# Performance work log

Measured on AMD Instinct MI355X. Metric: run time of the kernel, lower is better.

Reference implementation:

```python
import jax, jax.numpy as jnp
import numpy as np
from jax import lax

DN = ('NCHW', 'OIHW', 'NCHW')

def _conv(x, w, b, stride, pad):
    y = lax.conv_general_dilated(x, w, (stride, stride), [(pad, pad), (pad, pad)], dimension_numbers=DN)
    return y + b[None, :, None, None]

def _resblock(x, w1, b1, w2, b2, wd, bd, stride):
    # standard pre-activation-free ResNet block: conv3x3(stride)-ReLU-conv3x3 + 1x1(stride) skip, final ReLU
    identity = _conv(x, wd, bd, stride, 0)
    h = jax.nn.relu(_conv(x, w1, b1, stride, 1))
    h = _conv(h, w2, b2, 1, 1)
    return jax.nn.relu(h + identity)

def _deconv(x, w, b, stride, out_pad):
    # PyTorch ConvTranspose2d(k=3, padding=1, output_padding=out_pad) as dilated conv
    # w has PyTorch layout (in_ch, out_ch, kH, kW) -> flip spatially, swap to OIHW
    wt = jnp.flip(w, (2, 3)).transpose(1, 0, 2, 3)
    y = lax.conv_general_dilated(x, wt, (1, 1), [(1, 1 + out_pad), (1, 1 + out_pad)], lhs_dilation=(stride, stride), dimension_numbers=DN)
    return y + b[None, :, None, None]

def _quantize(enc, codebook):
    # enc: (B, C, H, W); codebook: (N, C). Squared-Euclidean distances, argmin, lookup.
    e = enc.transpose(0, 2, 3, 1)  # (B, H, W, C)
    d = (jnp.sum(e * e, axis=-1, keepdims=True)
         - 2.0 * jnp.einsum('bhwc,nc->bhwn', e, codebook)
         + jnp.sum(codebook * codebook, axis=-1))  # (B, H, W, N)
    idx = jnp.argmin(d, axis=-1)
    q = codebook[idx]  # (B, H, W, C)
    return q.transpose(0, 3, 1, 2)

def setup_inputs() -> dict:
    key = jax.random.key(0)
    ks = jax.random.split(key, 28)
    def W(k, shape):
        return jax.random.normal(k, shape, jnp.float32) * 0.05
    inp = {"x": jax.random.normal(ks[0], (32, 3, 256, 256), jnp.float32)}
    enc_chans = [(3, 64), (64, 128), (128, 64)]
    i = 1
    for l, (cin, cout) in enumerate(enc_chans):
        inp[f"enc{l}_w1"] = W(ks[i], (cout, cin, 3, 3))
        inp[f"enc{l}_b1"] = W(ks[i + 1], (cout,))
        inp[f"enc{l}_w2"] = W(ks[i + 2], (cout, cout, 3, 3))
        inp[f"enc{l}_b2"] = W(ks[i + 3], (cout,))
        inp[f"enc{l}_wd"] = W(ks[i + 4], (cout, cin, 1, 1))
        inp[f"enc{l}_bd"] = W(ks[i + 5], (cout,))
        i += 6
    # decoder ConvTranspose2d weights in PyTorch layout (in_ch, out_ch, 3, 3)
    dec_chans = [(64, 128), (128, 64), (64, 3)]
    for l, (cin, cout) in enumerate(dec_chans):
        inp[f"dec{l}_w"] = W(ks[i], (cin, cout, 3, 3))
        inp[f"dec{l}_b"] = W(ks[i + 1], (cout,))
        i += 2
    inp["codebook"] = W(ks[i], (512, 64))
    return inp

def reference(x, enc0_w1, enc0_b1, enc0_w2, enc0_b2, enc0_wd, enc0_bd,
              enc1_w1, enc1_b1, enc1_w2, enc1_b2, enc1_wd, enc1_bd,
              enc2_w1, enc2_b1, enc2_w2, enc2_b2, enc2_wd, enc2_bd,
              dec0_w, dec0_b, dec1_w, dec1_b, dec2_w, dec2_b, codebook):
    # encode: 256 -> 128 -> 64 -> 64 spatially
    h = _resblock(x, enc0_w1, enc0_b1, enc0_w2, enc0_b2, enc0_wd, enc0_bd, 2)
    h = _resblock(h, enc1_w1, enc1_b1, enc1_w2, enc1_b2, enc1_wd, enc1_bd, 2)
    h = _resblock(h, enc2_w1, enc2_b1, enc2_w2, enc2_b2, enc2_wd, enc2_bd, 1)
    q = _quantize(h, codebook)
    # decode with output_size matching encoder input shapes (output_padding: 0, 1, 1)
    h = jax.nn.relu(_deconv(q, dec0_w, dec0_b, 1, 0))   # 64 -> 64
    h = jax.nn.relu(_deconv(h, dec1_w, dec1_b, 2, 1))   # 64 -> 128
    return _deconv(h, dec2_w, dec2_b, 2, 1)             # 128 -> 256
```

## Files before the change

### kernel.cpp

```cpp
#include <hip/hip_runtime.h>
#include <cstddef>


typedef float v4f __attribute__((ext_vector_type(4)));
typedef _Float16 f16x8 __attribute__((ext_vector_type(8)));
typedef _Float16 f16x4 __attribute__((ext_vector_type(4)));

__device__ __forceinline__ void fma4(v4f& a, float p, const v4f& w) {
    a.x = fmaf(p, w.x, a.x); a.y = fmaf(p, w.y, a.y);
    a.z = fmaf(p, w.z, a.z); a.w = fmaf(p, w.w, a.w);
}

__global__ void repack_k(const float* __restrict__ src, float* __restrict__ dst,
                         int cout, int coutR, int cin, int flip, int deconv)
{
    int t = blockIdx.x * 256 + threadIdx.x;
    int tot = cin * 9 * cout;
    if (t >= tot) return;
    int co = t % cout; int k = (t / cout) % 9; int ci = t / (9 * cout);
    float v = 0.f;
    if (co < coutR) {
        int ks = flip ? 8 - k : k;
        v = deconv ? src[((size_t)ci * coutR + co) * 9 + ks]
                   : src[((size_t)co * cin + ci) * 9 + ks];
    }
    dst[t] = v;
}

__global__ void repackB16_k(const float* __restrict__ src, _Float16* __restrict__ bh,
                            _Float16* __restrict__ bl, int COUT, int CIN, int deconv)
{
    int t = blockIdx.x * 256 + threadIdx.x;
    int tot = 9 * CIN * COUT;
    if (t >= tot) return;
    int NGtot = COUT >> 4, C32 = CIN >> 5;
    int j = t & 7;
    int lane = (t >> 3) & 63;
    int blk = t >> 9;
    int ng = blk % NGtot; blk /= NGtot;
    int c32 = blk % C32;
    int tap = blk / C32;
    int co = ng * 16 + (lane & 15);
    int ci = c32 * 32 + ((lane >> 4) & 3) * 8 + j;
    float v = deconv ? src[((size_t)ci * COUT + co) * 9 + (8 - tap)]
                     : src[((size_t)co * CIN + ci) * 9 + tap];
    _Float16 h = (_Float16)v;
    _Float16 l = (_Float16)(v - (float)h);
    bh[t] = h; bl[t] = l;
}

__global__ void repackQ_k(const float* __restrict__ cb, _Float16* __restrict__ qb)
{
    int t = blockIdx.x * 256 + threadIdx.x;
    if (t >= 65536) return;
    int j = t & 7;
    int lane = (t >> 3) & 63;
    int hl = (t >> 9) & 1;
    int s = (t >> 10) & 1;
    int nt = t >> 11;
    int code = nt * 16 + (lane & 15);
    int ci = s * 32 + ((lane >> 4) & 3) * 8 + j;
    float v = cb[(size_t)code * 64 + ci];
    _Float16 h = (_Float16)v;
    qb[t] = hl ? (_Float16)(v - (float)h) : h;
}

__global__ void cbnorm_k(const float* __restrict__ cb, float* __restrict__ cn)
{
    int i = blockIdx.x * 256 + threadIdx.x;
    if (i >= 512) return;
    float s = 0.f;
#pragma unroll
    for (int j = 0; j < 64; ++j) { float v = cb[i * 64 + j]; s = fmaf(v, v, s); }
    cn[i] = s;
}

template<int CIN, bool RELU, int ADDMODE, bool CLIN, bool CLOUT>
__launch_bounds__(256, 2)
__global__ void mconv3s1_k(const float* __restrict__ in,
                           const _Float16* __restrict__ Bh, const _Float16* __restrict__ Bl,
                           const float* __restrict__ bias, float* __restrict__ out,
                           const float* __restrict__ addend,
                           int COUT, int H, int W)
{
    constexpr int C32 = CIN / 32;
    __shared__ __align__(16) unsigned char smBuf[76416];
    _Float16* AH = (_Float16*)smBuf;
    _Float16* AL = AH + 12960;
    _Float16* BW = AL + 12960;
    float* smO = (float*)smBuf;

    const int tid = threadIdx.x;
    const int lane = tid & 63, yb = tid >> 6;
    const int n16 = lane & 15, q = lane >> 4;

    int b = blockIdx.x;
    const int chunks = COUT >> 6;
    const int coch = b % chunks; b /= chunks;
    const int tX = W >> 4; const int tx = b % tX; b /= tX;
    const int tY = H >> 4; const int ty = b % tY; const int n = b / tY;
    const int x0 = tx * 16, y0 = ty * 16;
    const int NGtot = COUT >> 4;
    const int ngbase = coch * 4, cobase = coch * 64;

    v4f acc[4][4];
#pragma unroll
    for (int ng = 0; ng < 4; ++ng) {
        float bb = bias[cobase + ng * 16 + n16];
        v4f bv = {bb, bb, bb, bb};
#pragma unroll
        for (int mg = 0; mg < 4; ++mg) acc[mg][ng] = bv;
    }

    for (int c32 = 0; c32 < C32; ++c32) {
        __syncthreads();
        if (CLIN) {
            for (int u = tid; u < 2592; u += 256) {
                int cell = u >> 3, f4 = u & 7;
                int yy = cell / 18, xx = cell - yy * 18;
                int gy = y0 - 1 + yy, gx = x0 - 1 + xx;
                float4 v = make_float4(0.f, 0.f, 0.f, 0.f);
                if (gy >= 0 && gy < H && gx >= 0 && gx < W)
                    v = *(const float4*)&in[(((size_t)n * H + gy) * W + gx) * CIN + c32 * 32 + f4 * 4];
                f16x4 h4, l4;
                h4[0] = (_Float16)v.x; l4[0] = (_Float16)(v.x - (float)h4[0]);
                h4[1] = (_Float16)v.y; l4[1] = (_Float16)(v.y - (float)h4[1]);
                h4[2] = (_Float16)v.z; l4[2] = (_Float16)(v.z - (float)h4[2]);
                h4[3] = (_Float16)v.w; l4[3] = (_Float16)(v.w - (float)h4[3]);
                int a = (yy * 18 + xx) * 40 + f4 * 4;
                *(f16x4*)&AH[a] = h4; *(f16x4*)&AL[a] = l4;
            }
        } else {
            for (int u = tid; u < 10368; u += 256) {
                int ci = u / 324, rem = u - ci * 324;
                int yy = rem / 18, xx = rem - yy * 18;
                int gy = y0 - 1 + yy, gx = x0 - 1 + xx;
                float v = 0.f;
                if (gy >= 0 && gy < H && gx >= 0 && gx < W)
                    v = in[(((size_t)n * CIN + c32 * 32 + ci) * H + gy) * W + gx];
                _Float16 h = (_Float16)v;
                _Float16 l = (_Float16)(v - (float)h);
                int a = (yy * 18 + xx) * 40 + ci;
                AH[a] = h; AL[a] = l;
            }
        }
        for (int ky = 0; ky < 3; ++ky) {
            __syncthreads();
            for (int u = tid; u < 1536; u += 256) {
                int lu = u & 63;
                int rest = u >> 6;
                int hl = rest & 1; rest >>= 1;
                int ng = rest & 3;
                int tapL = rest >> 2;
                const uint4* srcp = (const uint4*)(hl ? Bl : Bh);
                size_t sidx = (((size_t)(ky * 3 + tapL) * C32 + c32) * NGtot + ngbase + ng) * 64 + lu;
                ((uint4*)BW)[u] = srcp[sidx];
            }
            __syncthreads();
#pragma unroll
            for (int kx = 0; kx < 3; ++kx) {
                f16x8 aH[4], aL[4];
#pragma unroll
                for (int mg = 0; mg < 4; ++mg) {
                    int aoff = ((4 * yb + mg + ky) * 18 + n16 + kx) * 40 + q * 8;
                    aH[mg] = *(const f16x8*)&AH[aoff];
                    aL[mg] = *(const f16x8*)&AL[aoff];
                }
                __builtin_amdgcn_s_setprio(1);
#pragma unroll
                for (int ng = 0; ng < 4; ++ng) {
                    int boff = ((kx * 4 + ng) * 2) * 512 + lane * 8;
                    f16x8 bH = *(const f16x8*)&BW[boff];
                    f16x8 bL = *(const f16x8*)&BW[boff + 512];
#pragma unroll
                    for (int mg = 0; mg < 4; ++mg) {
                        acc[mg][ng] = __builtin_amdgcn_mfma_f32_16x16x32_f16(aH[mg], bH, acc[mg][ng], 0, 0, 0);
                        acc[mg][ng] = __builtin_amdgcn_mfma_f32_16x16x32_f16(aL[mg], bH, acc[mg][ng], 0, 0, 0);
                        acc[mg][ng] = __builtin_amdgcn_mfma_f32_16x16x32_f16(aH[mg], bL, acc[mg][ng], 0, 0, 0);
                    }
                }
                __builtin_amdgcn_s_setprio(0);
            }
        }
    }

    __syncthreads();
#pragma unroll
    for (int mg = 0; mg < 4; ++mg)
#pragma unroll
        for (int ng = 0; ng < 4; ++ng) {
            int p = (4 * yb + mg) * 16 + q * 4;
            int co = ng * 16 + n16;
#pragma unroll
            for (int r = 0; r < 4; ++r)
                smO[co * 257 + p + r] = acc[mg][ng][r];
        }
    __syncthreads();
    if (CLOUT) {
        const int p = tid;
        const int py = p >> 4, px = p & 15;
        size_t cellBase = (((size_t)n * H + (y0 + py)) * W + (x0 + px)) * COUT + cobase;
        float* cellp = out + cellBase;
        const float* acell = (ADDMODE == 2) ? addend + cellBase : nullptr;
#pragma unroll
        for (int g = 0; g < 16; ++g) {
            float4 v;
            v.x = smO[(4 * g + 0) * 257 + p];
            v.y = smO[(4 * g + 1) * 257 + p];
            v.z = smO[(4 * g + 2) * 257 + p];
            v.w = smO[(4 * g + 3) * 257 + p];
            if (ADDMODE == 2) {
                float4 a4 = *(const float4*)&acell[4 * g];
                v.x += a4.x; v.y += a4.y; v.z += a4.z; v.w += a4.w;
            }
            if (RELU) {
                v.x = fmaxf(v.x, 0.f); v.y = fmaxf(v.y, 0.f);
                v.z = fmaxf(v.z, 0.f); v.w = fmaxf(v.w, 0.f);
            }
            *(float4*)&cellp[4 * g] = v;
        }
    } else {
        const size_t plane = (size_t)H * W;
        float* ob = out + ((size_t)n * COUT + cobase) * plane;
        const float* ab = (ADDMODE == 1) ? addend + ((size_t)n * COUT + cobase) * plane : nullptr;
#pragma unroll
        for (int k = 0; k < 64; ++k) {
            int e = tid + 256 * k;
            int co = e >> 8, p = e & 255;
            int py = p >> 4, px = p & 15;
            size_t g = (size_t)co * plane + (size_t)(y0 + py) * W + x0 + px;
            float v = smO[co * 257 + p];
            if (ADDMODE == 1) v += ab[g];
            if (RELU) v = fmaxf(v, 0.f);
            ob[g] = v;
        }
    }
}

template<int CIN, int NG, bool RELU>
__launch_bounds__(256, 3)
__global__ void mconv3s2_k(const float* __restrict__ in,
                           const _Float16* __restrict__ Bh, const _Float16* __restrict__ Bl,
                           const float* __restrict__ bias, float* __restrict__ out,
                           int COUT, int Hin, int Win)
{
    constexpr int C32 = CIN / 32;
    constexpr int ASZ = 9 * 2 * 17 * 40;
    __shared__ __align__(16) unsigned char smBuf[2 * ASZ * 2];
    _Float16* AH = (_Float16*)smBuf;
    _Float16* AL = AH + ASZ;
    float* smO = (float*)smBuf;

    const int tid = threadIdx.x;
    const int lane = tid & 63, yb = tid >> 6;
    const int n16 = lane & 15, q = lane >> 4;

    const int Hout = Hin >> 1, Wout = Win >> 1;
    int b = blockIdx.x;
    const int chunks = COUT / (NG * 16);
    const int coch = b % chunks; b /= chunks;
    const int tX = Wout >> 4; const int tx = b % tX; b /= tX;
    const int tY = Hout >> 2; const int ty = b % tY; const int n = b / tY;
    const int x0 = tx * 16, y0 = ty * 4;
    const int gx0 = 2 * x0 - 1, gy0 = 2 * y0 - 1;
    const int NGtot = COUT >> 4;
    const int ngbase = coch * NG, cobase = coch * NG * 16;

    v4f acc[NG];
#pragma unroll
    for (int ng = 0; ng < NG; ++ng) {
        float bb = bias[cobase + ng * 16 + n16];
        v4f bv = {bb, bb, bb, bb};
        acc[ng] = bv;
    }

    const uint4* bhp = (const uint4*)Bh;
    const uint4* blp = (const uint4*)Bl;

    for (int c32 = 0; c32 < C32; ++c32) {
        __syncthreads();
        for (int u = tid; u < 2376; u += 256) {
            int cell = u >> 3, f4 = u & 7;
            int yy = cell / 33, xx = cell - yy * 33;
            int gy = gy0 + yy, gx = gx0 + xx;
            float4 v = make_float4(0.f, 0.f, 0.f, 0.f);
            if (gy >= 0 && gy < Hin && gx >= 0 && gx < Win)
                v = *(const float4*)&in[(((size_t)n * Hin + gy) * Win + gx) * CIN + c32 * 32 + f4 * 4];
            f16x4 h4, l4;
            h4[0] = (_Float16)v.x; l4[0] = (_Float16)(v.x - (float)h4[0]);
            h4[1] = (_Float16)v.y; l4[1] = (_Float16)(v.y - (float)h4[1]);
            h4[2] = (_Float16)v.z; l4[2] = (_Float16)(v.z - (float)h4[2]);
            h4[3] = (_Float16)v.w; l4[3] = (_Float16)(v.w - (float)h4[3]);
            int a = ((yy * 2 + (xx & 1)) * 17 + (xx >> 1)) * 40 + f4 * 4;
            *(f16x4*)&AH[a] = h4; *(f16x4*)&AL[a] = l4;
        }
        __syncthreads();
#pragma unroll
        for (int ky = 0; ky < 3; ++ky) {
#pragma unroll
            for (int kx = 0; kx < 3; ++kx) {
                const int par = kx & 1, xs = kx >> 1;
                int aoff = (((2 * yb + ky) * 2 + par) * 17 + n16 + xs) * 40 + q * 8;
                f16x8 aH = *(const f16x8*)&AH[aoff];
                f16x8 aL = *(const f16x8*)&AL[aoff];
                size_t sb0 = (((size_t)(ky * 3 + kx) * C32 + c32) * NGtot + ngbase) * 64 + lane;
                __builtin_amdgcn_s_setprio(1);
#pragma unroll
                for (int ng = 0; ng < NG; ++ng) {
                    uint4 rH = bhp[sb0 + (size_t)ng * 64];
                    uint4 rL = blp[sb0 + (size_t)ng * 64];
                    f16x8 bH = *(const f16x8*)&rH;
                    f16x8 bL = *(const f16x8*)&rL;
                    acc[ng] = __builtin_amdgcn_mfma_f32_16x16x32_f16(aH, bH, acc[ng], 0, 0, 0);
                    acc[ng] = __builtin_amdgcn_mfma_f32_16x16x32_f16(aL, bH, acc[ng], 0, 0, 0);
                    acc[ng] = __builtin_amdgcn_mfma_f32_16x16x32_f16(aH, bL, acc[ng], 0, 0, 0);
                }
                __builtin_amdgcn_s_setprio(0);
            }
        }
    }

    __syncthreads();
#pragma unroll
    for (int ng = 0; ng < NG; ++ng) {
        int co = ng * 16 + n16;
        int p = yb * 16 + q * 4;
#pragma unroll
        for (int r = 0; r < 4; ++r)
            smO[co * 65 + p + r] = acc[ng][r];
    }
    __syncthreads();
    const int p2 = tid >> 2, s2 = tid & 3;
    const int py = p2 >> 4, px = p2 & 15;
    float* cellp = out + ((((size_t)n * Hout + (y0 + py)) * Wout + (x0 + px)) * COUT + s2 * 32);
#pragma unroll
    for (int k = 0; k < 8; ++k) {
        float4 v;
        v.x = smO[(s2 * 32 + 4 * k + 0) * 65 + p2];
        v.y = smO[(s2 * 32 + 4 * k + 1) * 65 + p2];
        v.z = smO[(s2 * 32 + 4 * k + 2) * 65 + p2];
        v.w = smO[(s2 * 32 + 4 * k + 3) * 65 + p2];
        if (RELU) {
            v.x = fmaxf(v.x, 0.f); v.y = fmaxf(v.y, 0.f);
            v.z = fmaxf(v.z, 0.f); v.w = fmaxf(v.w, 0.f);
        }
        *(float4*)&cellp[4 * k] = v;
    }
}

template<int CIN, bool RELU>
__launch_bounds__(256, 3)
__global__ void mdeconv2_k(const float* __restrict__ in,
                           const _Float16* __restrict__ Bh, const _Float16* __restrict__ Bl,
                           const float* __restrict__ bias, float* __restrict__ out,
                           int COUT, int Hin, int Win)
{
    constexpr int C32 = CIN / 32;
    __shared__ __align__(16) unsigned char smBuf[38976];
    _Float16* AH = (_Float16*)smBuf;
    _Float16* AL = AH + 3600;
    _Float16* BW = AL + 3600;
    float* smO = (float*)smBuf;

    const int tid = threadIdx.x;
    const int lane = tid & 63, yb = tid >> 6;
    const int n16 = lane & 15, q = lane >> 4;

    int b = blockIdx.x;
    const int chunks = COUT >> 6;
    const int coch = b % chunks; b /= chunks;
    const int tX = Win >> 4; const int tx = b % tX; b /= tX;
    const int tY = Hin >> 2; const int ty = b % tY; const int n = b / tY;
    const int x0 = tx * 16, y0 = ty * 4;
    const int NGtot = COUT >> 4;
    const int ngbase = coch * 4, cobase = coch * 64;

    v4f acc[4][4];
#pragma unroll
    for (int ng = 0; ng < 4; ++ng) {
        float bb = bias[cobase + ng * 16 + n16];
        v4f bv = {bb, bb, bb, bb};
#pragma unroll
        for (int ph = 0; ph < 4; ++ph) acc[ph][ng] = bv;
    }

    for (int c32 = 0; c32 < C32; ++c32) {
        __syncthreads();
        for (int u = tid; u < 680; u += 256) {
            int cell = u >> 3, f4 = u & 7;
            int yy = cell / 17, xx = cell - yy * 17;
            int gy = y0 + yy, gx = x0 + xx;
            float4 v = make_float4(0.f, 0.f, 0.f, 0.f);
            if (gy < Hin && gx < Win)
                v = *(const float4*)&in[(((size_t)n * Hin + gy) * Win + gx) * CIN + c32 * 32 + f4 * 4];
            f16x4 h4, l4;
            h4[0] = (_Float16)v.x; l4[0] = (_Float16)(v.x - (float)h4[0]);
            h4[1] = (_Float16)v.y; l4[1] = (_Float16)(v.y - (float)h4[1]);
            h4[2] = (_Float16)v.z; l4[2] = (_Float16)(v.z - (float)h4[2]);
            h4[3] = (_Float16)v.w; l4[3] = (_Float16)(v.w - (float)h4[3]);
            int a = (yy * 18 + xx) * 40 + f4 * 4;
            *(f16x4*)&AH[a] = h4; *(f16x4*)&AL[a] = l4;
        }
        for (int ky = 0; ky < 3; ++ky) {
            __syncthreads();
            for (int u = tid; u < 1536; u += 256) {
                int lu = u & 63;
                int rest = u >> 6;
                int hl = rest & 1; rest >>= 1;
                int ng = rest & 3;
                int tapL = rest >> 2;
                const uint4* srcp = (const uint4*)(hl ? Bl : Bh);
                size_t sidx = (((size_t)(ky * 3 + tapL) * C32 + c32) * NGtot + ngbase + ng) * 64 + lu;
                ((uint4*)BW)[u] = srcp[sidx];
            }
            __syncthreads();
            const int iy = (ky == 2) ? 1 : 0;
            const int phy = (ky == 1) ? 0 : 2;
#pragma unroll
            for (int kx = 0; kx < 3; ++kx) {
                const int ix = (kx == 2) ? 1 : 0;
                const int ph = phy + ((kx == 1) ? 0 : 1);
                int aoff = ((yb + iy) * 18 + n16 + ix) * 40 + q * 8;
                f16x8 aH = *(const f16x8*)&AH[aoff];
                f16x8 aL = *(const f16x8*)&AL[aoff];
                __builtin_amdgcn_s_setprio(1);
#pragma unroll
                for (int ng = 0; ng < 4; ++ng) {
                    int boff = ((kx * 4 + ng) * 2) * 512 + lane * 8;
                    f16x8 bH = *(const f16x8*)&BW[boff];
                    f16x8 bL = *(const f16x8*)&BW[boff + 512];
                    acc[ph][ng] = __builtin_amdgcn_mfma_f32_16x16x32_f16(aH, bH, acc[ph][ng], 0, 0, 0);
                    acc[ph][ng] = __builtin_amdgcn_mfma_f32_16x16x32_f16(aL, bH, acc[ph][ng], 0, 0, 0);
                    acc[ph][ng] = __builtin_amdgcn_mfma_f32_16x16x32_f16(aH, bL, acc[ph][ng], 0, 0, 0);
                }
                __builtin_amdgcn_s_setprio(0);
            }
        }
    }

    const int Wout = Win * 2;
    const size_t plane = (size_t)(Hin * 2) * (size_t)Wout;
    float* ob = out + ((size_t)n * COUT + cobase) * plane;
    const int oy0 = 2 * y0, ox0 = 2 * x0;
#pragma unroll
    for (int half = 0; half < 2; ++half) {
        __syncthreads();
#pragma unroll
        for (int ph = 0; ph < 4; ++ph) {
            const int dy = ph >> 1, dx = ph & 1;
#pragma unroll
            for (int g = 0; g < 2; ++g) {
                int ng = half * 2 + g;
#pragma unroll
                for (int r = 0; r < 4; ++r)
                    smO[(g * 16 + n16) * 257 + (2 * yb + dy) * 32 + 2 * (q * 4 + r) + dx] = acc[ph][ng][r];
            }
        }
        __syncthreads();
#pragma unroll
        for (int k = 0; k < 32; ++k) {
            int pos = tid;
            int oyl = pos >> 5, oxl = pos & 31;
            float v = smO[k * 257 + pos];
            if (RELU) v = fmaxf(v, 0.f);
            ob[(size_t)(half * 32 + k) * plane + (size_t)(oy0 + oyl) * Wout + ox0 + oxl] = v;
        }
    }
}

template<int CIN, int CB, bool RELU>
__launch_bounds__(256, 4)
__global__ void conv3s2_k(const float* __restrict__ in, const float* __restrict__ wp,
                          const float* __restrict__ bias, float* __restrict__ out,
                          int COUT, int Hin, int Win)
{
    constexpr int COC = 32;
    __shared__ float smIn[CB * 2178];
    __shared__ float smW[CB * 9 * COC];
    const int Hout = Hin >> 1, Wout = Win >> 1;
    const int tid = threadIdx.x;
    int b = blockIdx.x;
    const int chunks = COUT / COC;
    const int tX = Wout / 32, tY = Hout / 16;
    const int ch = b % chunks; b /= chunks;
    const int tx = b % tX; b /= tX;
    const int ty = b % tY; const int n = b / tY;
    const int cobase = ch * COC;
    const int r = tid >> 4, c = tid & 15;
    const int gy0 = ty * 32 - 1, gx0 = tx * 64 - 1;

    v4f acc[16];
#pragma unroll
    for (int g = 0; g < 8; ++g) {
        v4f bv = *(const v4f*)&bias[cobase + 4 * g];
        acc[g] = bv; acc[8 + g] = bv;
    }

    const size_t plane = (size_t)Hin * Win;
    const float* ip0 = in + (size_t)n * CIN * plane;
    const float* wp0 = wp + cobase;

    for (int ci0 = 0; ci0 < CIN; ci0 += CB) {
        __syncthreads();
        for (int idx = tid; idx < CB * 2178; idx += 256) {
            int ci = idx / 2178, rem = idx - ci * 2178;
            int rr = rem / 66, cc = rem - rr * 66;
            int gy = gy0 + rr, gx = gx0 + cc;
            float v = 0.f;
            if (gy >= 0 && gy < Hin && gx >= 0 && gx < Win)
                v = ip0[(size_t)(ci0 + ci) * plane + (size_t)gy * Win + gx];
            smIn[idx] = v;
        }
        for (int idx = tid; idx < CB * 9 * COC; idx += 256) {
            int q2 = idx >> 5, co = idx & 31;
            smW[idx] = wp0[((size_t)ci0 * 9 + q2) * COUT + co];
        }
        __syncthreads();

#pragma unroll 1
        for (int ci = 0; ci < CB; ++ci) {
            float p[15];
            const float* sp = &smIn[ci * 2178 + 2 * r * 66 + 4 * c];
#pragma unroll
            for (int i = 0; i < 3; ++i)
#pragma unroll
                for (int j = 0; j < 5; ++j)
                    p[i * 5 + j] = sp[i * 66 + j];
            const float* wrow = &smW[ci * 288];
#pragma unroll
            for (int k = 0; k < 9; ++k) {
                const int ky = k / 3, kx = k % 3;
#pragma unroll
                for (int g = 0; g < 8; ++g) {
                    v4f wv = *(const v4f*)&wrow[k * 32 + 4 * g];
                    fma4(acc[g],     p[ky * 5 + kx],     wv);
                    fma4(acc[8 + g], p[ky * 5 + kx + 2], wv);
                }
            }
        }
    }

    const int oy = ty * 16 + r, ox = tx * 32 + 2 * c;
    size_t cellBase = (((size_t)n * Hout + oy) * Wout + ox) * COUT + cobase;
#pragma unroll
    for (int g = 0; g < 8; ++g) {
        v4f v0 = acc[g], v1 = acc[8 + g];
        if (RELU) {
#pragma unroll
            for (int e = 0; e < 4; ++e) { v0[e] = fmaxf(v0[e], 0.f); v1[e] = fmaxf(v1[e], 0.f); }
        }
        *(v4f*)&out[cellBase + 4 * g] = v0;
        *(v4f*)&out[cellBase + COUT + 4 * g] = v1;
    }
}

template<int CIN, int CB, int COC, bool RELU>
__launch_bounds__(256, 3)
__global__ void deconv2_k(const float* __restrict__ in, const float* __restrict__ wp,
                          const float* __restrict__ bias, float* __restrict__ out,
                          int COUTR, int COUTP, int Hin, int Win)
{
    constexpr int RW = 33, RH = 17;
    __shared__ float smIn[CB * RH * RW];
    __shared__ float smW[CB * 9 * COC];
    const int Wout = Win * 2;
    const int tid = threadIdx.x;
    int b = blockIdx.x;
    const int chunks = COUTP / COC;
    const int qTX = Win / 32, qTY = Hin / 16;
    const int ch = b % chunks; b /= chunks;
    const int qtx = b % qTX; b /= qTX;
    const int qty = b % qTY; const int n = b / qTY;
    const int cobase = ch * COC;
    const int tqy = tid >> 4, tqx = tid & 15;
    const int qby = qty * 16, qbx = qtx * 32;

    v4f acc[8 * COC / 4];
#pragma unroll
    for (int g = 0; g < COC / 4; ++g) {
        v4f bv;
#pragma unroll
        for (int e = 0; e < 4; ++e)
            bv[e] = (cobase + 4 * g + e < COUTR) ? bias[cobase + 4 * g + e] : 0.f;
#pragma unroll
        for (int pt = 0; pt < 8; ++pt) acc[pt * (COC / 4) + g] = bv;
    }

    const size_t plane = (size_t)Hin * Win;
    const float* ip0 = in + (size_t)n * CIN * plane;
    const float* wp0 = wp + cobase;

    for (int ci0 = 0; ci0 < CIN; ci0 += CB) {
        __syncthreads();
        for (int idx = tid; idx < CB * RH * RW; idx += 256) {
            int ci = idx / (RH * RW), rem = idx - ci * (RH * RW);
            int rr = rem / RW, cc = rem - rr * RW;
            int gy = qby + rr, gx = qbx + cc;
            float v = 0.f;
            if (gy < Hin && gx < Win)
                v = ip0[(size_t)(ci0 + ci) * plane + (size_t)gy * Win + gx];
            smIn[idx] = v;
        }
        for (int idx = tid; idx < CB * 9 * COC; idx += 256) {
            int q2 = idx / COC, co = idx % COC;
            smW[idx] = wp0[((size_t)ci0 * 9 + q2) * COUTP + co];
        }
        __syncthreads();

#pragma unroll 1
        for (int ci = 0; ci < CB; ++ci) {
            float p[6];
            const float* sp = &smIn[ci * RH * RW + tqy * RW + 2 * tqx];
#pragma unroll
            for (int i = 0; i < 2; ++i)
#pragma unroll
                for (int j = 0; j < 3; ++j)
                    p[i * 3 + j] = sp[i * RW + j];
            const float* wrow = &smW[ci * 9 * COC];
#pragma unroll
            for (int k = 0; k < 9; ++k) {
                const int ky = k / 3, kx = k % 3;
                const int dy = (ky == 1) ? 0 : 1, iy = (ky == 0) ? 1 : 0;
                const int dx = (kx == 1) ? 0 : 1, ix = (kx == 0) ? 1 : 0;
#pragma unroll
                for (int g = 0; g < COC / 4; ++g) {
                    v4f wv = *(const v4f*)&wrow[k * COC + 4 * g];
                    fma4(acc[(0 + dy * 2 + dx) * (COC / 4) + g], p[iy * 3 + ix],     wv);
                    fma4(acc[(4 + dy * 2 + dx) * (COC / 4) + g], p[iy * 3 + ix + 1], wv);
                }
            }
        }
    }

    const size_t oPlane = (size_t)(Hin * 2) * Wout;
    const int oy = 2 * (qby + tqy), ox = 2 * (qbx + 2 * tqx);
#pragma unroll
    for (int g = 0; g < COC / 4; ++g)
#pragma unroll
        for (int e = 0; e < 4; ++e) {
            int cch = cobase + 4 * g + e;
            if (cch >= COUTR) break;
            float* op = out + ((size_t)n * COUTR + cch) * oPlane + (size_t)oy * Wout + ox;
#pragma unroll
            for (int a2 = 0; a2 < 2; ++a2) {
                float u0 = acc[(0 + a2 * 2 + 0) * (COC / 4) + g][e];
                float u1 = acc[(0 + a2 * 2 + 1) * (COC / 4) + g][e];
                float u2 = acc[(4 + a2 * 2 + 0) * (COC / 4) + g][e];
                float u3 = acc[(4 + a2 * 2 + 1) * (COC / 4) + g][e];
                if (RELU) { u0 = fmaxf(u0, 0.f); u1 = fmaxf(u1, 0.f);
                            u2 = fmaxf(u2, 0.f); u3 = fmaxf(u3, 0.f); }
                *(float4*)&op[(size_t)a2 * Wout] = make_float4(u0, u1, u2, u3);
            }
        }
}

template<int CIN, int S, bool RELU, bool CLIN, bool CLOUT>
__launch_bounds__(256, 4)
__global__ void conv1x1_k(const float* __restrict__ in, const float* __restrict__ w,
                          const float* __restrict__ bias, float* __restrict__ out,
                          int COUT, int Hin, int Win, int Hout, int Wout)
{
    constexpr int COC = 32;
    __shared__ float smW[CIN * COC];
    const int tid = threadIdx.x;
    int b = blockIdx.x;
    const int chunks = COUT / COC;
    const int spB = (Hout * Wout) / 256;
    const int ch = b % chunks; b /= chunks;
    const int sb = b % spB; const int n = b / spB;
    const int cobase = ch * COC;

    for (int idx = tid; idx < CIN * COC; idx += 256) {
        int ci = idx / COC, co = idx - ci * COC;
        smW[idx] = w[(size_t)(cobase + co) * CIN + ci];
    }
    __syncthreads();

    const int pos = sb * 256 + tid;
    const int oy = pos / Wout, ox = pos - oy * Wout;

    v4f acc[8];
#pragma unroll
    for (int g = 0; g < 8; ++g) acc[g] = *(const v4f*)&bias[cobase + 4 * g];

    if (CLIN) {
        const float* ip = in + (((size_t)n * Hin + oy * S) * Win + ox * S) * CIN;
#pragma unroll 1
        for (int c4 = 0; c4 < CIN / 4; ++c4) {
            v4f v = *(const v4f*)&ip[c4 * 4];
#pragma unroll
            for (int e = 0; e < 4; ++e)
#pragma unroll
                for (int g = 0; g < 8; ++g)
                    fma4(acc[g], v[e], *(const v4f*)&smW[(c4 * 4 + e) * COC + 4 * g]);
        }
    } else {
        const size_t inPlane = (size_t)Hin * Win;
        const float* ip = in + (size_t)n * CIN * inPlane + (size_t)(oy * S) * Win + (size_t)(ox * S);
#pragma unroll 1
        for (int ci = 0; ci < CIN; ++ci) {
            float v = ip[(size_t)ci * inPlane];
#pragma unroll
            for (int g = 0; g < 8; ++g)
                fma4(acc[g], v, *(const v4f*)&smW[ci * COC + 4 * g]);
        }
    }
    const size_t outPlane = (size_t)Hout * Wout;
    if (CLOUT) {
        size_t cb2 = ((size_t)n * outPlane + pos) * COUT + cobase;
#pragma unroll
        for (int g = 0; g < 8; ++g) {
            v4f v = acc[g];
            if (RELU) {
#pragma unroll
                for (int e = 0; e < 4; ++e) v[e] = fmaxf(v[e], 0.f);
            }
            *(v4f*)&out[cb2 + 4 * g] = v;
        }
    } else {
        float* op = out + ((size_t)n * COUT + cobase) * outPlane + pos;
#pragma unroll
        for (int g = 0; g < 8; ++g)
#pragma unroll
            for (int e = 0; e < 4; ++e) {
                float v = acc[g][e];
                if (RELU) v = fmaxf(v, 0.f);
                op[(size_t)(4 * g + e) * outPlane] = v;
            }
    }
}

__launch_bounds__(256, 4)
__global__ void mquant_k(const float* __restrict__ h, const _Float16* __restrict__ QB,
                         const float* __restrict__ cn, const float* __restrict__ cb,
                         float* __restrict__ q)
{
    __shared__ __align__(16) _Float16 AF[2][8192];
    __shared__ float cns[512];
    __shared__ int bidxs[128];

    const int tid = threadIdx.x;
    const int lane = tid & 63;
    const int wv = tid >> 6;
    const int n16 = lane & 15, qq = lane >> 4;

    const int n = blockIdx.x >> 5;
    const int rem0 = (blockIdx.x & 31) << 7;

    for (int u = tid; u < 1024; u += 256) {
        int posL = u >> 3, grp = u & 7;
        const float* gp = h + ((size_t)n * 4096 + rem0 + posL) * 64 + grp * 8;
        float4 v0 = *(const float4*)gp;
        float4 v1 = *(const float4*)(gp + 4);
        f16x8 hh, ll;
        hh[0] = (_Float16)v0.x; ll[0] = (_Float16)(v0.x - (float)hh[0]);
        hh[1] = (_Float16)v0.y; ll[1] = (_Float16)(v0.y - (float)hh[1]);
        hh[2] = (_Float16)v0.z; ll[2] = (_Float16)(v0.z - (float)hh[2]);
        hh[3] = (_Float16)v0.w; ll[3] = (_Float16)(v0.w - (float)hh[3]);
        hh[4] = (_Float16)v1.x; ll[4] = (_Float16)(v1.x - (float)hh[4]);
        hh[5] = (_Float16)v1.y; ll[5] = (_Float16)(v1.y - (float)hh[5]);
        hh[6] = (_Float16)v1.z; ll[6] = (_Float16)(v1.z - (float)hh[6]);
        hh[7] = (_Float16)v1.w; ll[7] = (_Float16)(v1.w - (float)hh[7]);
        int mt = posL >> 4, s = grp >> 2, qv = grp & 3;
        int a = ((mt * 2 + s) * 64 + (posL & 15) + qv * 16) * 8;
        *(f16x8*)&AF[0][a] = hh;
        *(f16x8*)&AF[1][a] = ll;
    }
    for (int u = tid; u < 512; u += 256) cns[u] = cn[u];
    __syncthreads();

    f16x8 aH[2][2], aL[2][2];
#pragma unroll
    for (int m = 0; m < 2; ++m)
#pragma unroll
        for (int s = 0; s < 2; ++s) {
            int a = (((wv * 2 + m) * 2 + s) * 64 + lane) * 8;
            aH[m][s] = *(const f16x8*)&AF[0][a];
            aL[m][s] = *(const f16x8*)&AF[1][a];
        }

    float best[2][4]; int bi[2][4];
#pragma unroll
    for (int m = 0; m < 2; ++m)
#pragma unroll
        for (int r = 0; r < 4; ++r) { best[m][r] = 3.4e38f; bi[m][r] = 0; }

    const uint4* qbp = (const uint4*)QB;
#pragma unroll 1
    for (int nt = 0; nt < 32; ++nt) {
        uint4 rH0 = qbp[((nt * 2 + 0) * 2 + 0) * 64 + lane];
        uint4 rL0 = qbp[((nt * 2 + 0) * 2 + 1) * 64 + lane];
        uint4 rH1 = qbp[((nt * 2 + 1) * 2 + 0) * 64 + lane];
        uint4 rL1 = qbp[((nt * 2 + 1) * 2 + 1) * 64 + lane];
        f16x8 bH0 = *(const f16x8*)&rH0;
        f16x8 bL0 = *(const f16x8*)&rL0;
        f16x8 bH1 = *(const f16x8*)&rH1;
        f16x8 bL1 = *(const f16x8*)&rL1;
        float cnv = cns[nt * 16 + n16];
        const int code = nt * 16 + n16;
        __builtin_amdgcn_s_setprio(1);
#pragma unroll
        for (int m = 0; m < 2; ++m) {
            v4f acc = {0.f, 0.f, 0.f, 0.f};
            acc = __builtin_amdgcn_mfma_f32_16x16x32_f16(aH[m][0], bH0, acc, 0, 0, 0);
            acc = __builtin_amdgcn_mfma_f32_16x16x32_f16(aL[m][0], bH0, acc, 0, 0, 0);
            acc = __builtin_amdgcn_mfma_f32_16x16x32_f16(aH[m][0], bL0, acc, 0, 0, 0);
            acc = __builtin_amdgcn_mfma_f32_16x16x32_f16(aH[m][1], bH1, acc, 0, 0, 0);
            acc = __builtin_amdgcn_mfma_f32_16x16x32_f16(aL[m][1], bH1, acc, 0, 0, 0);
            acc = __builtin_amdgcn_mfma_f32_16x16x32_f16(aH[m][1], bL1, acc, 0, 0, 0);
#pragma unroll
            for (int r = 0; r < 4; ++r) {
                float d = fmaf(-2.f, acc[r], cnv);
                if (d < best[m][r]) { best[m][r] = d; bi[m][r] = code; }
            }
        }
        __builtin_amdgcn_s_setprio(0);
    }

#pragma unroll
    for (int m = 0; m < 2; ++m)
#pragma unroll
        for (int r = 0; r < 4; ++r) {
#pragma unroll
            for (int msk = 1; msk < 16; msk <<= 1) {
                float ob = __shfl_xor(best[m][r], msk);
                int oi = __shfl_xor(bi[m][r], msk);
                if (ob < best[m][r] || (ob == best[m][r] && oi < bi[m][r])) {
                    best[m][r] = ob; bi[m][r] = oi;
                }
            }
            if (n16 == 0) bidxs[wv * 32 + m * 16 + qq * 4 + r] = bi[m][r];
        }
    __syncthreads();

    const int p = tid & 127, jh = tid >> 7;
    const int code = bidxs[p];
    const float4* crow4 = (const float4*)(cb + (size_t)code * 64);
    float4* qp4 = (float4*)(q + ((size_t)n * 4096 + rem0 + p) * 64);
#pragma unroll
    for (int k = 0; k < 8; ++k)
        qp4[jh * 8 + k] = crow4[jh * 8 + k];
}

extern "C" void kernel_launch(void* const* d_in, const int* in_sizes, int n_in,
                              void* d_out, int out_size, void* d_ws, size_t ws_size,
                              hipStream_t stream)
{
    const float* x    = (const float*)d_in[0];
    const float* e0w1 = (const float*)d_in[1];  const float* e0b1 = (const float*)d_in[2];
    const float* e0w2 = (const float*)d_in[3];  const float* e0b2 = (const float*)d_in[4];
    const float* e0wd = (const float*)d_in[5];  const float* e0bd = (const float*)d_in[6];
    const float* e1w1 = (const float*)d_in[7];  const float* e1b1 = (const float*)d_in[8];
    const float* e1w2 = (const float*)d_in[9];  const float* e1b2 = (const float*)d_in[10];
    const float* e1wd = (const float*)d_in[11]; const float* e1bd = (const float*)d_in[12];
    const float* e2w1 = (const float*)d_in[13]; const float* e2b1 = (const float*)d_in[14];
    const float* e2w2 = (const float*)d_in[15]; const float* e2b2 = (const float*)d_in[16];
    const float* e2wd = (const float*)d_in[17]; const float* e2bd = (const float*)d_in[18];
    const float* d0w  = (const float*)d_in[19]; const float* d0b  = (const float*)d_in[20];
    const float* d1w  = (const float*)d_in[21]; const float* d1b  = (const float*)d_in[22];
    const float* d2w  = (const float*)d_in[23]; const float* d2b  = (const float*)d_in[24];
    const float* cb   = (const float*)d_in[25];
    float* out = (float*)d_out;
    float* ws  = (float*)d_ws;

    float* P_e0w1 = out + 0;
    _Float16* Bh_d1   = (_Float16*)(out + 1728);
    _Float16* Bl_d1   = (_Float16*)(out + 38592);
    _Float16* Bh_e0c2 = (_Float16*)(out + 77760);
    _Float16* Bl_e0c2 = (_Float16*)(out + 96192);
    _Float16* Bh_e1c2 = (_Float16*)(out + 114624);
    _Float16* Bl_e1c2 = (_Float16*)(out + 188352);
    _Float16* Bh_e2c1 = (_Float16*)(out + 262080);
    _Float16* Bl_e2c1 = (_Float16*)(out + 298944);
    _Float16* Bh_e2c2 = (_Float16*)(out + 335808);
    _Float16* Bl_e2c2 = (_Float16*)(out + 354240);
    _Float16* Bh_d0   = (_Float16*)(out + 372672);
    _Float16* Bl_d0   = (_Float16*)(out + 409536);
    _Float16* Bh_e1c1 = (_Float16*)(out + 446400);
    _Float16* Bl_e1c1 = (_Float16*)(out + 483264);
    _Float16* QB = (_Float16*)(out + 520128);
    float* CN = out + 552896;
    float* P_d2w  = ws + 50405376;

    float* S0 = ws;
    float* T1 = ws + 33554432;
    float* T3 = ws + 33554432;
    float* S1 = ws + 50331648;
    float* S2 = ws;
    float* T5 = ws + 8388608;
    float* Q  = ws + 16777216;
    float* D0 = ws + 33554432;
    float* D1 = ws;

    dim3 blk(256);
    auto rp = [&](const float* src, float* dst, int cout, int coutR, int cin, int flip, int dec) {
        int tot = cin * 9 * cout;
        repack_k<<<dim3((tot + 255) / 256), blk, 0, stream>>>(src, dst, cout, coutR, cin, flip, dec);
    };
    auto rpB = [&](const float* src, _Float16* bh, _Float16* bl, int cout, int cin, int dec) {
        int tot = 9 * cin * cout;
        repackB16_k<<<dim3((tot + 255) / 256), blk, 0, stream>>>(src, bh, bl, cout, cin, dec);
    };

    rp(e0w1, P_e0w1, 64, 64, 3, 0, 0);
    rpB(e0w2, Bh_e0c2, Bl_e0c2, 64, 64, 0);
    rpB(e1w1, Bh_e1c1, Bl_e1c1, 128, 64, 0);
    rpB(e1w2, Bh_e1c2, Bl_e1c2, 128, 128, 0);
    rpB(e2w1, Bh_e2c1, Bl_e2c1, 64, 128, 0);
    rpB(e2w2, Bh_e2c2, Bl_e2c2, 64, 64, 0);
    rpB(d0w,  Bh_d0,   Bl_d0,   128, 64, 1);
    rpB(d1w,  Bh_d1,   Bl_d1,   64, 128, 1);
    repackQ_k<<<dim3(256), blk, 0, stream>>>(cb, QB);
    cbnorm_k<<<dim3(2), blk, 0, stream>>>(cb, CN);

    conv1x1_k<3, 2, false, false, true><<<dim3(32 * 64 * 2), blk, 0, stream>>>(
        x, e0wd, e0bd, S0, 64, 256, 256, 128, 128);
    conv3s2_k<3, 3, true><<<dim3(32 * 8 * 4 * 2), blk, 0, stream>>>(
        x, P_e0w1, e0b1, T1, 64, 256, 256);
    mconv3s1_k<64, true, 2, true, true><<<dim3(32 * 8 * 8 * 1), blk, 0, stream>>>(
        T1, Bh_e0c2, Bl_e0c2, e0b2, S0, S0, 64, 128, 128);

    conv1x1_k<64, 2, false, true, true><<<dim3(32 * 16 * 4), blk, 0, stream>>>(
        S0, e1wd, e1bd, S1, 128, 128, 128, 64, 64);
    mconv3s2_k<64, 8, true><<<dim3(32 * 16 * 4), blk, 0, stream>>>(
        S0, Bh_e1c1, Bl_e1c1, e1b1, T3, 128, 128, 128);
    mconv3s1_k<128, true, 2, true, true><<<dim3(32 * 4 * 4 * 2), blk, 0, stream>>>(
        T3, Bh_e1c2, Bl_e1c2, e1b2, S1, S1, 128, 64, 64);

    conv1x1_k<128, 1, false, true, true><<<dim3(32 * 16 * 2), blk, 0, stream>>>(
        S1, e2wd, e2bd, S2, 64, 64, 64, 64, 64);
    mconv3s1_k<128, true, 0, true, true><<<dim3(32 * 4 * 4 * 1), blk, 0, stream>>>(
        S1, Bh_e2c1, Bl_e2c1, e2b1, T5, nullptr, 64, 64, 64);
    rp(d2w, P_d2w, 4, 3, 64, 0, 1);
    mconv3s1_k<64, true, 2, true, true><<<dim3(32 * 4 * 4 * 1), blk, 0, stream>>>(
        T5, Bh_e2c2, Bl_e2c2, e2b2, S2, S2, 64, 64, 64);

    mquant_k<<<dim3(1024), blk, 0, stream>>>(S2, QB, CN, cb, Q);

    mconv3s1_k<64, true, 0, true, true><<<dim3(32 * 4 * 4 * 2), blk, 0, stream>>>(
        Q, Bh_d0, Bl_d0, d0b, D0, nullptr, 128, 64, 64);

    mdeconv2_k<128, true><<<dim3(32 * 16 * 4), blk, 0, stream>>>(
        D0, Bh_d1, Bl_d1, d1b, D1, 64, 64, 64);

    deconv2_k<64, 8, 4, false><<<dim3(32 * 4 * 8), blk, 0, stream>>>(
        D1, P_d2w, d2b, out, 3, 4, 128, 128);
}
```

Baseline: 1.453 ms.

## Fuse strided 1x1 skip convolutions into the stride-2 3x3 conv kernels

Removes the two standalone conv1x1 launches for the encoder skip paths in blocks 0 and 1. The skip result is now computed inside the stride-2 3x3 conv kernels, reusing the input tile already staged in shared memory: the center tap's A fragment feeds extra MFMAs with repacked fp16 hi/lo 1x1 weights, and the scalar conv3s2 path does FMAs from a small shared weight array. This avoids re-reading S0 and x from global memory. The cost is more registers and accumulators per thread (accW[8] in mconv3s2), which may hurt occupancy, plus a second shared-memory transpose and store pass in the epilogue.

```diff
diff --git a/kernel.cpp b/kernel.cpp
--- a/kernel.cpp
+++ b/kernel.cpp
@@ -49,6 +49,25 @@
     bh[t] = h; bl[t] = l;
 }
 
+__global__ void repackW16_k(const float* __restrict__ src, _Float16* __restrict__ wh,
+                            _Float16* __restrict__ wl, int COUT, int CIN)
+{
+    int t = blockIdx.x * 256 + threadIdx.x;
+    int tot = CIN * COUT;
+    if (t >= tot) return;
+    int NGtot = COUT >> 4;
+    int j = t & 7;
+    int lane = (t >> 3) & 63;
+    int blk = t >> 9;
+    int ng = blk % NGtot;
+    int c32 = blk / NGtot;
+    int co = ng * 16 + (lane & 15);
+    int ci = c32 * 32 + ((lane >> 4) & 3) * 8 + j;
+    float v = src[(size_t)co * CIN + ci];
+    _Float16 h = (_Float16)v;
+    wh[t] = h; wl[t] = (_Float16)(v - (float)h);
+}
+
 __global__ void repackQ_k(const float* __restrict__ cb, _Float16* __restrict__ qb)
 {
     int t = blockIdx.x * 256 + threadIdx.x;
@@ -242,6 +261,8 @@
 __global__ void mconv3s2_k(const float* __restrict__ in,
                            const _Float16* __restrict__ Bh, const _Float16* __restrict__ Bl,
                            const float* __restrict__ bias, float* __restrict__ out,
+                           const _Float16* __restrict__ Wh, const _Float16* __restrict__ Wl,
+                           const float* __restrict__ bias1, float* __restrict__ out1,
                            int COUT, int Hin, int Win)
 {
     constexpr int C32 = CIN / 32;
@@ -267,15 +288,21 @@
     const int ngbase = coch * NG, cobase = coch * NG * 16;
 
     v4f acc[NG];
+    v4f accW[NG];
 #pragma unroll
     for (int ng = 0; ng < NG; ++ng) {
         float bb = bias[cobase + ng * 16 + n16];
         v4f bv = {bb, bb, bb, bb};
         acc[ng] = bv;
+        float bw = bias1[cobase + ng * 16 + n16];
+        v4f bwv = {bw, bw, bw, bw};
+        accW[ng] = bwv;
     }
 
     const uint4* bhp = (const uint4*)Bh;
     const uint4* blp = (const uint4*)Bl;
+    const uint4* whp = (const uint4*)Wh;
+    const uint4* wlp = (const uint4*)Wl;
 
     for (int c32 = 0; c32 < C32; ++c32) {
         __syncthreads();
@@ -316,6 +343,21 @@
                     acc[ng] = __builtin_amdgcn_mfma_f32_16x16x32_f16(aH, bL, acc[ng], 0, 0, 0);
                 }
                 __builtin_amdgcn_s_setprio(0);
+                if (ky == 1 && kx == 1) {
+                    size_t sw0 = ((size_t)c32 * NGtot + ngbase) * 64 + lane;
+                    __builtin_amdgcn_s_setprio(1);
+#pragma unroll
+                    for (int ng = 0; ng < NG; ++ng) {
+                        uint4 rH = whp[sw0 + (size_t)ng * 64];
+                        uint4 rL = wlp[sw0 + (size_t)ng * 64];
+                        f16x8 bH = *(const f16x8*)&rH;
+                        f16x8 bL = *(const f16x8*)&rL;
+                        accW[ng] = __builtin_amdgcn_mfma_f32_16x16x32_f16(aH, bH, accW[ng], 0, 0, 0);
+                        accW[ng] = __builtin_amdgcn_mfma_f32_16x16x32_f16(aL, bH, accW[ng], 0, 0, 0);
+                        accW[ng] = __builtin_amdgcn_mfma_f32_16x16x32_f16(aH, bL, accW[ng], 0, 0, 0);
+                    }
+                    __builtin_amdgcn_s_setprio(0);
+                }
             }
         }
     }
@@ -345,6 +387,27 @@
             v.z = fmaxf(v.z, 0.f); v.w = fmaxf(v.w, 0.f);
         }
         *(float4*)&cellp[4 * k] = v;
+    }
+
+    __syncthreads();
+#pragma unroll
+    for (int ng = 0; ng < NG; ++ng) {
+        int co = ng * 16 + n16;
+        int p = yb * 16 + q * 4;
+#pragma unroll
+        for (int r = 0; r < 4; ++r)
+            smO[co * 65 + p + r] = accW[ng][r];
+    }
+    __syncthreads();
+    float* cellp1 = out1 + ((((size_t)n * Hout + (y0 + py)) * Wout + (x0 + px)) * COUT + s2 * 32);
+#pragma unroll
+    for (int k = 0; k < 8; ++k) {
+        float4 v;
+        v.x = smO[(s2 * 32 + 4 * k + 0) * 65 + p2];
+        v.y = smO[(s2 * 32 + 4 * k + 1) * 65 + p2];
+        v.z = smO[(s2 * 32 + 4 * k + 2) * 65 + p2];
+        v.w = smO[(s2 * 32 + 4 * k + 3) * 65 + p2];
+        *(float4*)&cellp1[4 * k] = v;
     }
 }
 
@@ -468,15 +531,18 @@
     }
 }
 
-template<int CIN, int CB, bool RELU>
+template<int CIN, int CB, bool RELU, bool FUSE>
 __launch_bounds__(256, 4)
 __global__ void conv3s2_k(const float* __restrict__ in, const float* __restrict__ wp,
                           const float* __restrict__ bias, float* __restrict__ out,
+                          const float* __restrict__ wd, const float* __restrict__ bd,
+                          float* __restrict__ out1,
                           int COUT, int Hin, int Win)
 {
     constexpr int COC = 32;
     __shared__ float smIn[CB * 2178];
     __shared__ float smW[CB * 9 * COC];
+    __shared__ float smWD[96];
     const int Hout = Hin >> 1, Wout = Win >> 1;
     const int tid = threadIdx.x;
     int b = blockIdx.x;
@@ -515,6 +581,10 @@
             int q2 = idx >> 5, co = idx & 31;
             smW[idx] = wp0[((size_t)ci0 * 9 + q2) * COUT + co];
         }
+        if (FUSE && tid < 96) {
+            int ci = tid >> 5, co = tid & 31;
+            smWD[tid] = wd[(size_t)(cobase + co) * 3 + ci];
+        }
         __syncthreads();
 
 #pragma unroll 1
@@ -551,6 +621,32 @@
         }
         *(v4f*)&out[cellBase + 4 * g] = v0;
         *(v4f*)&out[cellBase + COUT + 4 * g] = v1;
+    }
+
+    if (FUSE) {
+        v4f a0[8], a1[8];
+#pragma unroll
+        for (int g = 0; g < 8; ++g) {
+            v4f bv = *(const v4f*)&bd[cobase + 4 * g];
+            a0[g] = bv; a1[g] = bv;
+        }
+#pragma unroll
+        for (int ci = 0; ci < CB; ++ci) {
+            const float* sp = &smIn[ci * 2178 + 2 * r * 66 + 4 * c];
+            float v0 = sp[66 + 1], v1 = sp[66 + 3];
+#pragma unroll
+            for (int g = 0; g < 8; ++g) {
+                v4f wv = *(const v4f*)&smWD[ci * 32 + 4 * g];
+                fma4(a0[g], v0, wv);
+                fma4(a1[g], v1, wv);
+            }
+        }
+        size_t cb1 = (((size_t)n * Hout + oy) * Wout + ox) * COUT + cobase;
+#pragma unroll
+        for (int g = 0; g < 8; ++g) {
+            *(v4f*)&out1[cb1 + 4 * g] = a0[g];
+            *(v4f*)&out1[cb1 + COUT + 4 * g] = a1[g];
+        }
     }
 }
 
@@ -880,6 +976,8 @@
     _Float16* Bl_e1c1 = (_Float16*)(out + 483264);
     _Float16* QB = (_Float16*)(out + 520128);
     float* CN = out + 552896;
+    _Float16* Wh_e1d = (_Float16*)(out + 553408);
+    _Float16* Wl_e1d = (_Float16*)(out + 557504);
     float* P_d2w  = ws + 50405376;
 
     float* S0 = ws;
@@ -910,20 +1008,17 @@
     rpB(e2w2, Bh_e2c2, Bl_e2c2, 64, 64, 0);
     rpB(d0w,  Bh_d0,   Bl_d0,   128, 64, 1);
     rpB(d1w,  Bh_d1,   Bl_d1,   64, 128, 1);
+    repackW16_k<<<dim3(32), blk, 0, stream>>>(e1wd, Wh_e1d, Wl_e1d, 128, 64);
     repackQ_k<<<dim3(256), blk, 0, stream>>>(cb, QB);
     cbnorm_k<<<dim3(2), blk, 0, stream>>>(cb, CN);
 
-    conv1x1_k<3, 2, false, false, true><<<dim3(32 * 64 * 2), blk, 0, stream>>>(
-        x, e0wd, e0bd, S0, 64, 256, 256, 128, 128);
-    conv3s2_k<3, 3, true><<<dim3(32 * 8 * 4 * 2), blk, 0, stream>>>(
-        x, P_e0w1, e0b1, T1, 64, 256, 256);
+    conv3s2_k<3, 3, true, true><<<dim3(32 * 8 * 4 * 2), blk, 0, stream>>>(
+        x, P_e0w1, e0b1, T1, e0wd, e0bd, S0, 64, 256, 256);
     mconv3s1_k<64, true, 2, true, true><<<dim3(32 * 8 * 8 * 1), blk, 0, stream>>>(
         T1, Bh_e0c2, Bl_e0c2, e0b2, S0, S0, 64, 128, 128);
 
-    conv1x1_k<64, 2, false, true, true><<<dim3(32 * 16 * 4), blk, 0, stream>>>(
-        S0, e1wd, e1bd, S1, 128, 128, 128, 64, 64);
     mconv3s2_k<64, 8, true><<<dim3(32 * 16 * 4), blk, 0, stream>>>(
-        S0, Bh_e1c1, Bl_e1c1, e1b1, T3, 128, 128, 128);
+        S0, Bh_e1c1, Bl_e1c1, e1b1, T3, Wh_e1d, Wl_e1d, e1bd, S1, 128, 128, 128);
     mconv3s1_k<128, true, 2, true, true><<<dim3(32 * 4 * 4 * 2), blk, 0, stream>>>(
         T3, Bh_e1c2, Bl_e1c2, e1b2, S1, S1, 128, 64, 64);
 
```

New measurement: 1.309 ms. 1.11x faster.
